# Performance work log

Measured on AMD Instinct MI355X. Metric: run time of the kernel, lower is better.

The kernel has to match this reference:

```python
import jax, jax.numpy as jnp
import numpy as np

N = 100_000      # nodes
NNZ = 3_200_000  # nonzeros in precomputed mediator Laplacian (avg degree 32)
D, H1, H2, C = 512, 32, 16, 40  # h = [512, 2**5, 2**4, 40] per HyperGCN init with l=3


def _hyper_conv(H, W, b, row, col, w, n):
    """One HyperGraphConvolution (fast mode): A @ (H @ W) + b with COO sparse A."""
    HW = H @ W                              # [n, out] dense transform
    msg = HW[col] * w[:, None]              # gather source rows, scale by edge weight
    agg = jax.ops.segment_sum(msg, row, num_segments=n)  # scatter-add to destinations
    return agg + b


def setup_inputs() -> dict:
    key = jax.random.key(0)
    ks = jax.random.split(key, 8)

    def glorot(k, a, b):
        s = jnp.sqrt(6.0 / (a + b)).astype(jnp.float32)
        return jax.random.uniform(k, (a, b), minval=-s, maxval=s, dtype=jnp.float32)

    return {
        "x": jax.random.normal(ks[0], (N, D), dtype=jnp.float32),
        "edge_row": jax.random.randint(ks[1], (NNZ,), 0, N, dtype=jnp.int32),
        "edge_col": jax.random.randint(ks[2], (NNZ,), 0, N, dtype=jnp.int32),
        "edge_weight": jax.random.uniform(ks[3], (NNZ,), dtype=jnp.float32),
        "W0": glorot(ks[4], D, H1), "b0": jnp.zeros((H1,), jnp.float32),
        "W1": glorot(ks[5], H1, H2), "b1": jnp.zeros((H2,), jnp.float32),
        "W2": glorot(ks[6], H2, C), "b2": jnp.zeros((C,), jnp.float32),
    }


def reference(x, edge_row, edge_col, edge_weight, W0, b0, W1, b1, W2, b2):
    n = x.shape[0]
    H = x
    # l-layer HyperGCN: relu(conv) each layer; dropout between layers is identity in eval mode
    for (W, b) in ((W0, b0), (W1, b1), (W2, b2)):
        H = jax.nn.relu(_hyper_conv(H, W, b, edge_row, edge_col, edge_weight, n))
    return H
```

## Files before the change

### kernel.cpp

```cpp
#include <hip/hip_runtime.h>
#include <cstdint>

#define D_IN 512
#define HID1 32
#define HID2 16
#define C_OUT 40


__global__ __launch_bounds__(256) void k_hist(const int* __restrict__ row,
                                              int* __restrict__ cnt, int nnz) {
  int i = blockIdx.x * 256 + threadIdx.x;
  if (i < nnz) atomicAdd(&cnt[row[i]], 1);
}

__global__ __launch_bounds__(256) void k_scan1(const int* __restrict__ cnt,
                                               int* __restrict__ bsum, int n) {
  __shared__ int sd[256];
  int t = threadIdx.x;
  int i = blockIdx.x * 256 + t;
  sd[t] = (i < n) ? cnt[i] : 0;
  __syncthreads();
  for (int s = 128; s > 0; s >>= 1) {
    if (t < s) sd[t] += sd[t + s];
    __syncthreads();
  }
  if (t == 0) bsum[blockIdx.x] = sd[0];
}

__global__ __launch_bounds__(1024) void k_scan2(int* __restrict__ bsum, int nb) {
  __shared__ int sd[1024];
  int t = threadIdx.x;
  int v = (t < nb) ? bsum[t] : 0;
  sd[t] = v;
  __syncthreads();
  for (int s = 1; s < 1024; s <<= 1) {
    int tv = 0;
    if (t >= s) tv = sd[t - s];
    __syncthreads();
    if (t >= s) sd[t] += tv;
    __syncthreads();
  }
  if (t < nb) bsum[t] = sd[t] - v;
}

__global__ __launch_bounds__(256) void k_scan3(const int* __restrict__ cnt,
                                               const int* __restrict__ bsum,
                                               int* __restrict__ rp,
                                               int* __restrict__ pos,
                                               int n, int nnz) {
  __shared__ int sd[256];
  int t = threadIdx.x;
  int i = blockIdx.x * 256 + t;
  int v = (i < n) ? cnt[i] : 0;
  sd[t] = v;
  __syncthreads();
  for (int s = 1; s < 256; s <<= 1) {
    int tv = 0;
    if (t >= s) tv = sd[t - s];
    __syncthreads();
    if (t >= s) sd[t] += tv;
    __syncthreads();
  }
  int excl = sd[t] - v + bsum[blockIdx.x];
  if (i < n) { rp[i] = excl; pos[i] = excl; }
  if (i == n) rp[n] = nnz;
}

__global__ __launch_bounds__(256) void k_scatter(const int* __restrict__ row,
                                                 const int* __restrict__ col,
                                                 const float* __restrict__ w,
                                                 int* __restrict__ pos,
                                                 int2* __restrict__ cpk, int nnz) {
  int i = blockIdx.x * 256 + threadIdx.x;
  if (i < nnz) {
    int p = atomicAdd(&pos[row[i]], 1);
    cpk[p] = make_int2(col[i], __float_as_int(w[i]));
  }
}


#define FMA_ROW(i, xv)                                                     \
  acc[i][0] += xv.x * wv0.x + xv.y * wv1.x + xv.z * wv2.x + xv.w * wv3.x;  \
  acc[i][1] += xv.x * wv0.y + xv.y * wv1.y + xv.z * wv2.y + xv.w * wv3.y;  \
  acc[i][2] += xv.x * wv0.z + xv.y * wv1.z + xv.z * wv2.z + xv.w * wv3.z;  \
  acc[i][3] += xv.x * wv0.w + xv.y * wv1.w + xv.z * wv2.w + xv.w * wv3.w;

__global__ __launch_bounds__(256) void k_gemm1(const float* __restrict__ x,
                                               const float* __restrict__ W,
                                               float* __restrict__ out, int n) {
  __shared__ float xs[128 * 68];
  __shared__ float ws[64 * 32];
  const int tid = threadIdx.x;
  const int row0 = blockIdx.x * 128;
  const int c0 = (tid & 7) * 4;
  const int rs = tid >> 3;
  float acc[4][4] = {};
  for (int k0 = 0; k0 < D_IN; k0 += 64) {
#pragma unroll
    for (int j = 0; j < 8; ++j) {
      int l = tid + 256 * j;
      int r = l >> 4, p = (l & 15) * 4;
      float4 v = make_float4(0.f, 0.f, 0.f, 0.f);
      if (row0 + r < n)
        v = *(const float4*)(x + (size_t)(row0 + r) * D_IN + k0 + p);
      *(float4*)(xs + r * 68 + p) = v;
    }
#pragma unroll
    for (int j = 0; j < 2; ++j) {
      int l = tid + 256 * j;
      int kk = l >> 3, p = (l & 7) * 4;
      *(float4*)(ws + kk * 32 + p) = *(const float4*)(W + (size_t)(k0 + kk) * HID1 + p);
    }
    __syncthreads();
#pragma unroll
    for (int kk = 0; kk < 64; kk += 4) {
      float4 wv0 = *(const float4*)(ws + (kk + 0) * 32 + c0);
      float4 wv1 = *(const float4*)(ws + (kk + 1) * 32 + c0);
      float4 wv2 = *(const float4*)(ws + (kk + 2) * 32 + c0);
      float4 wv3 = *(const float4*)(ws + (kk + 3) * 32 + c0);
      float4 xv0 = *(const float4*)(xs + (rs + 0) * 68 + kk);
      float4 xv1 = *(const float4*)(xs + (rs + 32) * 68 + kk);
      float4 xv2 = *(const float4*)(xs + (rs + 64) * 68 + kk);
      float4 xv3 = *(const float4*)(xs + (rs + 96) * 68 + kk);
      FMA_ROW(0, xv0)
      FMA_ROW(1, xv1)
      FMA_ROW(2, xv2)
      FMA_ROW(3, xv3)
    }
    __syncthreads();
  }
#pragma unroll
  for (int i = 0; i < 4; ++i) {
    int r = row0 + rs + 32 * i;
    if (r < n) {
      float4 v = make_float4(acc[i][0], acc[i][1], acc[i][2], acc[i][3]);
      *(float4*)(out + (size_t)r * HID1 + c0) = v;
    }
  }
}


template <int IN, int OUT, bool PRE, bool POST>
__global__ __launch_bounds__(256) void k_gemm_small(const float* __restrict__ Hin,
                                                    const float* __restrict__ bpre,
                                                    const float* __restrict__ W,
                                                    const float* __restrict__ bpost,
                                                    float* __restrict__ out, int n) {
  int r = blockIdx.x * 256 + threadIdx.x;
  if (r >= n) return;
  float h[IN];
#pragma unroll
  for (int k = 0; k < IN; k += 4) {
    float4 v = *(const float4*)(Hin + (size_t)r * IN + k);
    if (PRE) {
      h[k + 0] = fmaxf(v.x + bpre[k + 0], 0.f);
      h[k + 1] = fmaxf(v.y + bpre[k + 1], 0.f);
      h[k + 2] = fmaxf(v.z + bpre[k + 2], 0.f);
      h[k + 3] = fmaxf(v.w + bpre[k + 3], 0.f);
    } else {
      h[k + 0] = v.x; h[k + 1] = v.y; h[k + 2] = v.z; h[k + 3] = v.w;
    }
  }
  float acc[OUT] = {};
#pragma unroll
  for (int k = 0; k < IN; ++k)
#pragma unroll
    for (int c = 0; c < OUT; ++c)
      acc[c] += h[k] * W[k * OUT + c];
#pragma unroll
  for (int c = 0; c < OUT; c += 4) {
    float4 v;
    if (POST) {
      v = make_float4(fmaxf(acc[c] + bpost[c], 0.f),
                      fmaxf(acc[c + 1] + bpost[c + 1], 0.f),
                      fmaxf(acc[c + 2] + bpost[c + 2], 0.f),
                      fmaxf(acc[c + 3] + bpost[c + 3], 0.f));
    } else {
      v = make_float4(acc[c], acc[c + 1], acc[c + 2], acc[c + 3]);
    }
    *(float4*)(out + (size_t)r * OUT + c) = v;
  }
}


template <int COLS, bool EPI>
__global__ __launch_bounds__(256) void k_spmm(const int* __restrict__ rp,
                                              const int2* __restrict__ cpk,
                                              const float* __restrict__ HW,
                                              const float* __restrict__ bias,
                                              float* __restrict__ out, int n) {
  constexpr int RPW = 64 / COLS;
  const int lane = threadIdx.x & 63;
  const int wid = (blockIdx.x * blockDim.x + threadIdx.x) >> 6;
  const int sub = lane / COLS;
  const int c = lane % COLS;
  const int r = wid * RPW + sub;
  if (r >= n) return;
  const int s = rp[r], e = rp[r + 1];
  float acc = 0.f;
  int i = s;
  for (; i + 4 <= e; i += 4) {
    int2 p0 = cpk[i + 0];
    int2 p1 = cpk[i + 1];
    int2 p2 = cpk[i + 2];
    int2 p3 = cpk[i + 3];
    float v0 = HW[(size_t)p0.x * COLS + c];
    float v1 = HW[(size_t)p1.x * COLS + c];
    float v2 = HW[(size_t)p2.x * COLS + c];
    float v3 = HW[(size_t)p3.x * COLS + c];
    acc = fmaf(v0, __int_as_float(p0.y), acc);
    acc = fmaf(v1, __int_as_float(p1.y), acc);
    acc = fmaf(v2, __int_as_float(p2.y), acc);
    acc = fmaf(v3, __int_as_float(p3.y), acc);
  }
  for (; i < e; ++i) {
    int2 p = cpk[i];
    acc = fmaf(HW[(size_t)p.x * COLS + c], __int_as_float(p.y), acc);
  }
  if (EPI) acc = fmaxf(acc + bias[c], 0.f);
  out[(size_t)r * COLS + c] = acc;
}


extern "C" void kernel_launch(void* const* d_in, const int* in_sizes, int n_in,
                              void* d_out, int out_size, void* d_ws, size_t ws_size,
                              hipStream_t stream) {
  const float* x  = (const float*)d_in[0];
  const int* erow = (const int*)d_in[1];
  const int* ecol = (const int*)d_in[2];
  const float* ew = (const float*)d_in[3];
  const float* W0 = (const float*)d_in[4];
  const float* b0 = (const float*)d_in[5];
  const float* W1 = (const float*)d_in[6];
  const float* b1 = (const float*)d_in[7];
  const float* W2 = (const float*)d_in[8];
  const float* b2 = (const float*)d_in[9];
  float* out = (float*)d_out;

  const int n = in_sizes[0] / D_IN;
  const int nnz = in_sizes[1];

  char* ws = (char*)d_ws;
  float* A  = (float*)(ws + 0);
  float* B  = (float*)(ws + 16000000);
  int* cnt  = (int*)(ws + 28800000);
  int* rp   = (int*)(ws + 29200000);
  int* pos  = (int*)(ws + 29600064);
  int* bsum = (int*)(ws + 30000064);
  int2* cpk = (int2*)(ws + 30003200);

  const int nb = (n + 255) / 256;
  const int eb = (nnz + 255) / 256;

  hipMemsetAsync(cnt, 0, (size_t)n * 4, stream);
  k_hist<<<eb, 256, 0, stream>>>(erow, cnt, nnz);
  k_scan1<<<nb, 256, 0, stream>>>(cnt, bsum, n);
  k_scan2<<<1, 1024, 0, stream>>>(bsum, nb);
  k_scan3<<<nb, 256, 0, stream>>>(cnt, bsum, rp, pos, n, nnz);
  k_scatter<<<eb, 256, 0, stream>>>(erow, ecol, ew, pos, cpk, nnz);

  k_gemm1<<<(n + 127) / 128, 256, 0, stream>>>(x, W0, A, n);
  k_spmm<HID1, false><<<(n + 7) / 8, 256, 0, stream>>>(rp, cpk, A, nullptr, B, n);

  k_gemm_small<HID1, HID2, true, false>
      <<<(n + 255) / 256, 256, 0, stream>>>(B, b0, W1, nullptr, A, n);
  k_spmm<HID2, true><<<(n + 15) / 16, 256, 0, stream>>>(rp, cpk, A, b1, B, n);

  k_spmm<HID2, false><<<(n + 15) / 16, 256, 0, stream>>>(rp, cpk, B, nullptr, A, n);
  k_gemm_small<HID2, C_OUT, false, true>
      <<<(n + 255) / 256, 256, 0, stream>>>(A, nullptr, W2, b2, out, n);
}
```

Baseline: 1.036 ms.

## Double-buffer GEMM1 with direct global-to-LDS loads and unroll SpMM gathers

The first dense transform now stages x and W tiles into shared memory with global_load_lds in 32-wide K chunks. It double-buffers the tiles so the next chunk loads while the current one is computed, and uses an XOR swizzle in place of padding to avoid bank conflicts. The SpMM inner loop gains an 8-way unrolled path that issues more independent gathers before accumulating, to raise memory-level parallelism. The risks are correctness of the swizzle and async-load synchronization, plus extra register pressure in the SpMM kernel.

```diff
diff --git a/kernel.cpp b/kernel.cpp
--- a/kernel.cpp
+++ b/kernel.cpp
@@ -5,6 +5,11 @@
 #define HID1 32
 #define HID2 16
 #define C_OUT 40
+
+#define GLOAD_LDS16(gp, lp)                                                     \
+  __builtin_amdgcn_global_load_lds(                                             \
+      (__attribute__((address_space(1))) const void*)(gp),                      \
+      (__attribute__((address_space(3))) void*)(lp), 16, 0, 0)
 
 
 __global__ __launch_bounds__(256) void k_hist(const int* __restrict__ row,
@@ -88,47 +93,55 @@
 __global__ __launch_bounds__(256) void k_gemm1(const float* __restrict__ x,
                                                const float* __restrict__ W,
                                                float* __restrict__ out, int n) {
-  __shared__ float xs[128 * 68];
-  __shared__ float ws[64 * 32];
+  __shared__ float xs[2][128 * 32];
+  __shared__ float ws[2][32 * 32];
   const int tid = threadIdx.x;
   const int row0 = blockIdx.x * 128;
   const int c0 = (tid & 7) * 4;
   const int rs = tid >> 3;
+  const int xsw = (rs & 7) << 4;
+  const int wvb = (tid & 192) * 4;
   float acc[4][4] = {};
-  for (int k0 = 0; k0 < D_IN; k0 += 64) {
-#pragma unroll
-    for (int j = 0; j < 8; ++j) {
-      int l = tid + 256 * j;
-      int r = l >> 4, p = (l & 15) * 4;
-      float4 v = make_float4(0.f, 0.f, 0.f, 0.f);
-      if (row0 + r < n)
-        v = *(const float4*)(x + (size_t)(row0 + r) * D_IN + k0 + p);
-      *(float4*)(xs + r * 68 + p) = v;
-    }
-#pragma unroll
-    for (int j = 0; j < 2; ++j) {
-      int l = tid + 256 * j;
-      int kk = l >> 3, p = (l & 7) * 4;
-      *(float4*)(ws + kk * 32 + p) = *(const float4*)(W + (size_t)(k0 + kk) * HID1 + p);
-    }
-    __syncthreads();
-#pragma unroll
-    for (int kk = 0; kk < 64; kk += 4) {
-      float4 wv0 = *(const float4*)(ws + (kk + 0) * 32 + c0);
-      float4 wv1 = *(const float4*)(ws + (kk + 1) * 32 + c0);
-      float4 wv2 = *(const float4*)(ws + (kk + 2) * 32 + c0);
-      float4 wv3 = *(const float4*)(ws + (kk + 3) * 32 + c0);
-      float4 xv0 = *(const float4*)(xs + (rs + 0) * 68 + kk);
-      float4 xv1 = *(const float4*)(xs + (rs + 32) * 68 + kk);
-      float4 xv2 = *(const float4*)(xs + (rs + 64) * 68 + kk);
-      float4 xv3 = *(const float4*)(xs + (rs + 96) * 68 + kk);
+
+#define STAGE(b, k0)                                                         \
+  {                                                                          \
+    _Pragma("unroll") for (int j = 0; j < 4; ++j) {                          \
+      const int L = j * 4096 + tid * 16;          \
+      const int row = L >> 7;                                                \
+      const int src = (L & 127) ^ ((row & 7) << 4);                          \
+      int gr = row0 + row;                                                   \
+      gr = gr < n ? gr : n - 1;                                              \
+      const float* gp = x + (size_t)gr * D_IN + (k0) + (src >> 2);           \
+      GLOAD_LDS16(gp, xs[b] + j * 1024 + wvb);                               \
+    }                                                                        \
+    GLOAD_LDS16(W + (size_t)(k0)*HID1 + tid * 4, ws[b] + wvb);               \
+  }
+
+  STAGE(0, 0)
+  int cur = 0;
+  for (int t = 0; t < D_IN / 32; ++t) {
+    __syncthreads();
+    if (t + 1 < D_IN / 32) STAGE(cur ^ 1, (t + 1) * 32)
+    const float* wb = ws[cur];
+    const char* xb = (const char*)xs[cur];
+#pragma unroll
+    for (int kk = 0; kk < 32; kk += 4) {
+      float4 wv0 = *(const float4*)(wb + (kk + 0) * 32 + c0);
+      float4 wv1 = *(const float4*)(wb + (kk + 1) * 32 + c0);
+      float4 wv2 = *(const float4*)(wb + (kk + 2) * 32 + c0);
+      float4 wv3 = *(const float4*)(wb + (kk + 3) * 32 + c0);
+      float4 xv0 = *(const float4*)(xb + (rs + 0) * 128 + ((kk * 4) ^ xsw));
+      float4 xv1 = *(const float4*)(xb + (rs + 32) * 128 + ((kk * 4) ^ xsw));
+      float4 xv2 = *(const float4*)(xb + (rs + 64) * 128 + ((kk * 4) ^ xsw));
+      float4 xv3 = *(const float4*)(xb + (rs + 96) * 128 + ((kk * 4) ^ xsw));
       FMA_ROW(0, xv0)
       FMA_ROW(1, xv1)
       FMA_ROW(2, xv2)
       FMA_ROW(3, xv3)
     }
-    __syncthreads();
-  }
+    cur ^= 1;
+  }
+#undef STAGE
 #pragma unroll
   for (int i = 0; i < 4; ++i) {
     int r = row0 + rs + 32 * i;
@@ -199,11 +212,18 @@
   const int s = rp[r], e = rp[r + 1];
   float acc = 0.f;
   int i = s;
+  for (; i + 8 <= e; i += 8) {
+    int2 p[8];
+    float v[8];
+#pragma unroll
+    for (int u = 0; u < 8; ++u) p[u] = cpk[i + u];
+#pragma unroll
+    for (int u = 0; u < 8; ++u) v[u] = HW[(size_t)p[u].x * COLS + c];
+#pragma unroll
+    for (int u = 0; u < 8; ++u) acc = fmaf(v[u], __int_as_float(p[u].y), acc);
+  }
   for (; i + 4 <= e; i += 4) {
-    int2 p0 = cpk[i + 0];
-    int2 p1 = cpk[i + 1];
-    int2 p2 = cpk[i + 2];
-    int2 p3 = cpk[i + 3];
+    int2 p0 = cpk[i + 0], p1 = cpk[i + 1], p2 = cpk[i + 2], p3 = cpk[i + 3];
     float v0 = HW[(size_t)p0.x * COLS + c];
     float v1 = HW[(size_t)p1.x * COLS + c];
     float v2 = HW[(size_t)p2.x * COLS + c];
```

Result: faster. 911.3 us (-12.0%).
